# Optimization experiments

Hardware: AMD Instinct MI355X
Metric: run time of the kernel (lower is better)

Reference implementation:

```python
import jax, jax.numpy as jnp
import numpy as np

N = 100000   # nodes
E = 1600000  # edges
F_IN = 128
H = 128
C = 40


def setup_inputs() -> dict:
    key = jax.random.key(0)
    ks = jax.random.split(key, 8)
    x = jax.random.normal(ks[0], (N, F_IN), dtype=jnp.float32)
    edge_index = jax.random.randint(ks[1], (2, E), 0, N, dtype=jnp.int32)
    s_in = 1.0 / np.sqrt(F_IN)
    s_h = 1.0 / np.sqrt(H)
    w0 = jax.random.uniform(ks[2], (F_IN, H), jnp.float32, -s_in, s_in)
    b0 = jnp.zeros((H,), jnp.float32)
    w1 = jax.random.uniform(ks[3], (H, H), jnp.float32, -s_h, s_h)
    b1 = jnp.zeros((H,), jnp.float32)
    wl = jax.random.uniform(ks[4], (H, C), jnp.float32, -s_h, s_h)
    bl = jax.random.uniform(ks[5], (C,), jnp.float32, -s_h, s_h)
    return {"x": x, "edge_index": edge_index, "w0": w0, "b0": b0,
            "w1": w1, "b1": b1, "wl": wl, "bl": bl}


def gcn_conv(x, edge_index, w, b, n):
    # PyG GCNConv: linear transform, add self-loops, D^-1/2 A_hat D^-1/2 aggregation, + bias
    loops = jnp.arange(n, dtype=edge_index.dtype)
    src = jnp.concatenate([edge_index[0], loops])
    dst = jnp.concatenate([edge_index[1], loops])
    deg = jax.ops.segment_sum(jnp.ones_like(dst, dtype=x.dtype), dst, num_segments=n)
    dinv = jnp.where(deg > 0, jax.lax.rsqrt(jnp.maximum(deg, 1.0)), 0.0)
    norm = dinv[src] * dinv[dst]                      # [E+N]
    h = x @ w                                         # [N, out]
    out = jax.ops.segment_sum(norm[:, None] * h[src], dst, num_segments=n)
    return out + b


def reference(x, edge_index, w0, b0, w1, b1, wl, bl):
    # layer 0 (no residual: in/out dims differ conceptually at i==0)
    h = jax.nn.relu(gcn_conv(x, edge_index, w0, b0, N))
    # layer 1 with residual (shapes match); dropout is identity at inference
    h = jax.nn.relu(gcn_conv(h, edge_index, w1, b1, N)) + h
    return jax.nn.log_softmax(h @ wl + bl, axis=1)
```

## Files before the change

### kernel.cpp

```cpp
#include <hip/hip_runtime.h>
#include <math.h>

#define F 128
constexpr int BLK = 256;
constexpr int CAP = 64;

__device__ __forceinline__ unsigned short f2bf(float f) {
    unsigned int b = __float_as_uint(f);
    return (unsigned short)((b + 0x7fffu + ((b >> 16) & 1u)) >> 16);
}


__global__ void bucket_kernel(const int* __restrict__ src, const int* __restrict__ dst, int e,
                              int* __restrict__ counts, int* __restrict__ colb) {
    int i = blockIdx.x * BLK + threadIdx.x;
    if (i < e) {
        int d = dst[i];
        int r = atomicAdd(&counts[d], 1);
        if (r < CAP) colb[d * CAP + r] = src[i];
    }
}

__global__ void dinv_kernel(const int* __restrict__ counts, float* __restrict__ dinv, int n) {
    int i = blockIdx.x * BLK + threadIdx.x;
    if (i < n) dinv[i] = rsqrtf((float)(counts[i] + 1));
}


__global__ __launch_bounds__(256) void mm128_kernel(const float* __restrict__ A,
                                                    const float* __restrict__ W,
                                                    unsigned short* __restrict__ Cb, int n) {
    __shared__ float Ws[64 * 64];
    __shared__ float Xs[64 * 65];
    int t = threadIdx.x;
    int row0 = blockIdx.x * 64;
    int cb = blockIdx.y * 64;
    int r0 = (t & 15) * 4;
    int c0 = (t >> 4) * 4;
    float acc[4][4] = {};

    for (int kt = 0; kt < 2; ++kt) {
        if (kt) __syncthreads();
#pragma unroll
        for (int i = 0; i < 4; i++) {
            int chunk = t + i * 256;
            int k = chunk >> 4;
            int c = (chunk & 15) << 2;
            *(float4*)&Ws[k * 64 + c] = *(const float4*)&W[(kt * 64 + k) * 128 + cb + c];
        }
#pragma unroll
        for (int i = 0; i < 4; i++) {
            int chunk = t + i * 256;
            int r = chunk >> 4;
            int k4 = (chunk & 15) << 2;
            int gr = row0 + r;
            float4 v = (gr < n) ? *(const float4*)&A[(size_t)gr * 128 + kt * 64 + k4]
                                : make_float4(0.f, 0.f, 0.f, 0.f);
            Xs[r * 65 + k4 + 0] = v.x;
            Xs[r * 65 + k4 + 1] = v.y;
            Xs[r * 65 + k4 + 2] = v.z;
            Xs[r * 65 + k4 + 3] = v.w;
        }
        __syncthreads();

#pragma unroll 8
        for (int k = 0; k < 64; ++k) {
            float4 w = *(const float4*)&Ws[k * 64 + c0];
            float x0 = Xs[(r0 + 0) * 65 + k];
            float x1 = Xs[(r0 + 1) * 65 + k];
            float x2 = Xs[(r0 + 2) * 65 + k];
            float x3 = Xs[(r0 + 3) * 65 + k];
            acc[0][0] += x0 * w.x; acc[0][1] += x0 * w.y; acc[0][2] += x0 * w.z; acc[0][3] += x0 * w.w;
            acc[1][0] += x1 * w.x; acc[1][1] += x1 * w.y; acc[1][2] += x1 * w.z; acc[1][3] += x1 * w.w;
            acc[2][0] += x2 * w.x; acc[2][1] += x2 * w.y; acc[2][2] += x2 * w.z; acc[2][3] += x2 * w.w;
            acc[3][0] += x3 * w.x; acc[3][1] += x3 * w.y; acc[3][2] += x3 * w.z; acc[3][3] += x3 * w.w;
        }
    }
#pragma unroll
    for (int m = 0; m < 4; m++) {
        int gr = row0 + r0 + m;
        if (gr < n) {
            ushort4 o;
            o.x = f2bf(acc[m][0]); o.y = f2bf(acc[m][1]);
            o.z = f2bf(acc[m][2]); o.w = f2bf(acc[m][3]);
            *(ushort4*)&Cb[(size_t)gr * 128 + cb + c0] = o;
        }
    }
}


template <bool RESID>
__global__ __launch_bounds__(256) void gather_kernel(const unsigned int* __restrict__ hb,
                                                     const int* __restrict__ cntp,
                                                     const int* __restrict__ colb,
                                                     const float* __restrict__ dinv,
                                                     const float* __restrict__ bias,
                                                     const float* __restrict__ resid,
                                                     float* __restrict__ out, int n) {
    int node = blockIdx.x * 4 + (threadIdx.x >> 6);
    if (node >= n) return;
    int lane = threadIdx.x & 63;

    int cnt = min(cntp[node], CAP);
    int eb = node * CAP;
    float ax = 0.f, ay = 0.f;

    int idx = 0;
    float w = 0.f;
    if (lane < cnt) {
        idx = colb[eb + lane];
        w = dinv[idx];
    }
    int e = 0;
    for (; e + 8 <= cnt; e += 8) {
        int s0 = __shfl(idx, e + 0), s1 = __shfl(idx, e + 1);
        int s2 = __shfl(idx, e + 2), s3 = __shfl(idx, e + 3);
        int s4 = __shfl(idx, e + 4), s5 = __shfl(idx, e + 5);
        int s6 = __shfl(idx, e + 6), s7 = __shfl(idx, e + 7);
        float w0 = __shfl(w, e + 0), w1 = __shfl(w, e + 1);
        float w2 = __shfl(w, e + 2), w3 = __shfl(w, e + 3);
        float w4 = __shfl(w, e + 4), w5 = __shfl(w, e + 5);
        float w6 = __shfl(w, e + 6), w7 = __shfl(w, e + 7);
        unsigned int u0 = hb[(size_t)s0 * 64 + lane];
        unsigned int u1 = hb[(size_t)s1 * 64 + lane];
        unsigned int u2 = hb[(size_t)s2 * 64 + lane];
        unsigned int u3 = hb[(size_t)s3 * 64 + lane];
        unsigned int u4 = hb[(size_t)s4 * 64 + lane];
        unsigned int u5 = hb[(size_t)s5 * 64 + lane];
        unsigned int u6 = hb[(size_t)s6 * 64 + lane];
        unsigned int u7 = hb[(size_t)s7 * 64 + lane];
        ax += w0 * __uint_as_float(u0 << 16); ay += w0 * __uint_as_float(u0 & 0xffff0000u);
        ax += w1 * __uint_as_float(u1 << 16); ay += w1 * __uint_as_float(u1 & 0xffff0000u);
        ax += w2 * __uint_as_float(u2 << 16); ay += w2 * __uint_as_float(u2 & 0xffff0000u);
        ax += w3 * __uint_as_float(u3 << 16); ay += w3 * __uint_as_float(u3 & 0xffff0000u);
        ax += w4 * __uint_as_float(u4 << 16); ay += w4 * __uint_as_float(u4 & 0xffff0000u);
        ax += w5 * __uint_as_float(u5 << 16); ay += w5 * __uint_as_float(u5 & 0xffff0000u);
        ax += w6 * __uint_as_float(u6 << 16); ay += w6 * __uint_as_float(u6 & 0xffff0000u);
        ax += w7 * __uint_as_float(u7 << 16); ay += w7 * __uint_as_float(u7 & 0xffff0000u);
    }
    for (; e < cnt; ++e) {
        int s = __shfl(idx, e);
        float ww = __shfl(w, e);
        unsigned int u = hb[(size_t)s * 64 + lane];
        ax += ww * __uint_as_float(u << 16);
        ay += ww * __uint_as_float(u & 0xffff0000u);
    }

    float di = dinv[node];
    unsigned int us = hb[(size_t)node * 64 + lane];
    ax = di * (ax + di * __uint_as_float(us << 16));
    ay = di * (ay + di * __uint_as_float(us & 0xffff0000u));
    float2 bb = ((const float2*)bias)[lane];
    ax = fmaxf(ax + bb.x, 0.f);
    ay = fmaxf(ay + bb.y, 0.f);
    if (RESID) {
        float2 r = ((const float2*)resid)[(size_t)node * 64 + lane];
        ax += r.x;
        ay += r.y;
    }
    ((float2*)out)[(size_t)node * 64 + lane] = make_float2(ax, ay);
}


__global__ __launch_bounds__(256) void cls_kernel(const float* __restrict__ H,
                                                  const float* __restrict__ WL,
                                                  const float* __restrict__ BL,
                                                  float* __restrict__ out, int n) {
    __shared__ float Hs[64 * 132];
    __shared__ float WsP[128 * 48];
    __shared__ float Bs[40];
    int t = threadIdx.x;
    int n0 = blockIdx.x * 64;

    for (int i = t; i < 128 * 40; i += 256) {
        int k = i / 40;
        int c = i % 40;
        WsP[k * 48 + (c / 10) * 12 + (c % 10)] = WL[i];
    }
    if (t < 40) Bs[t] = BL[t];
#pragma unroll
    for (int i = 0; i < 8; i++) {
        int chunk = t + i * 256;
        int r = chunk >> 5;
        int kk = (chunk & 31) << 2;
        int gr = n0 + r;
        float4 v = (gr < n) ? *(const float4*)&H[(size_t)gr * 128 + kk]
                            : make_float4(0.f, 0.f, 0.f, 0.f);
        *(float4*)&Hs[r * 132 + kk] = v;
    }
    __syncthreads();

    int ln = t >> 2;
    int g = t & 3;
    int node = n0 + ln;
    float acc[10];
#pragma unroll
    for (int j = 0; j < 10; j++) acc[j] = 0.f;

    for (int k4 = 0; k4 < 128; k4 += 4) {
        float4 hv = *(const float4*)&Hs[ln * 132 + k4];
#pragma unroll
        for (int kk = 0; kk < 4; ++kk) {
            const float* wr = &WsP[(k4 + kk) * 48 + g * 12];
            float4 wa = *(const float4*)wr;
            float4 wb = *(const float4*)(wr + 4);
            float2 wc = *(const float2*)(wr + 8);
            float hvk = (&hv.x)[kk];
            acc[0] += hvk * wa.x; acc[1] += hvk * wa.y; acc[2] += hvk * wa.z; acc[3] += hvk * wa.w;
            acc[4] += hvk * wb.x; acc[5] += hvk * wb.y; acc[6] += hvk * wb.z; acc[7] += hvk * wb.w;
            acc[8] += hvk * wc.x; acc[9] += hvk * wc.y;
        }
    }
#pragma unroll
    for (int j = 0; j < 10; j++) acc[j] += Bs[g * 10 + j];

    float m = acc[0];
#pragma unroll
    for (int j = 1; j < 10; j++) m = fmaxf(m, acc[j]);
    m = fmaxf(m, __shfl_xor(m, 1, 64));
    m = fmaxf(m, __shfl_xor(m, 2, 64));
    float ssum = 0.f;
#pragma unroll
    for (int j = 0; j < 10; j++) ssum += expf(acc[j] - m);
    ssum += __shfl_xor(ssum, 1, 64);
    ssum += __shfl_xor(ssum, 2, 64);
    float ls = logf(ssum);

    if (node < n) {
#pragma unroll
        for (int j = 0; j < 10; j++) out[(size_t)node * 40 + g * 10 + j] = acc[j] - m - ls;
    }
}


extern "C" void kernel_launch(void* const* d_in, const int* in_sizes, int n_in,
                              void* d_out, int out_size, void* d_ws, size_t ws_size,
                              hipStream_t stream) {
    const float* x  = (const float*)d_in[0];
    const int*   ei = (const int*)d_in[1];
    const float* w0 = (const float*)d_in[2];
    const float* b0 = (const float*)d_in[3];
    const float* w1 = (const float*)d_in[4];
    const float* b1 = (const float*)d_in[5];
    const float* wl = (const float*)d_in[6];
    const float* bl = (const float*)d_in[7];
    float* out = (float*)d_out;

    int n = in_sizes[0] / F;
    int e = in_sizes[1] / 2;
    const int* src = ei;
    const int* dst = ei + e;

    char* ws = (char*)d_ws;
    size_t off = 0;
    auto alloc = [&](size_t bytes) {
        void* p = ws + off;
        off += (bytes + 255) & ~(size_t)255;
        return p;
    };
    unsigned short* B1b = (unsigned short*)alloc((size_t)n * F * 2);
    float*          B2  = (float*)alloc((size_t)n * F * 4);
    float*          dinv   = (float*)alloc((size_t)n * 4);
    int*            counts = (int*)alloc((size_t)n * 4);
    int*            colb   = (int*)alloc((size_t)n * CAP * 4);
    (void)ws_size;

    int nbN = (n + BLK - 1) / BLK;
    int nbE = (e + BLK - 1) / BLK;
    dim3 mmg((n + 63) / 64, 2);

    hipMemsetAsync(counts, 0, (size_t)n * 4, stream);
    bucket_kernel<<<nbE, BLK, 0, stream>>>(src, dst, e, counts, colb);
    dinv_kernel<<<nbN, BLK, 0, stream>>>(counts, dinv, n);

    mm128_kernel<<<mmg, BLK, 0, stream>>>(x, w0, B1b, n);
    gather_kernel<false><<<(n + 3) / 4, BLK, 0, stream>>>((const unsigned int*)B1b, counts, colb,
                                                          dinv, b0, nullptr, B2, n);
    mm128_kernel<<<mmg, BLK, 0, stream>>>(B2, w1, B1b, n);
    gather_kernel<true><<<(n + 3) / 4, BLK, 0, stream>>>((const unsigned int*)B1b, counts, colb,
                                                         dinv, b1, B2, B2, n);
    cls_kernel<<<(n + 63) / 64, BLK, 0, stream>>>(B2, wl, bl, out, n);
}
```

Measured before the change: 529.9 us.

## Fuse edge bucketing with first matmul and compute dinv inline in gather

```diff
diff --git a/kernel.cpp b/kernel.cpp
--- a/kernel.cpp
+++ b/kernel.cpp
@@ -11,19 +11,82 @@
 }
 
 
-__global__ void bucket_kernel(const int* __restrict__ src, const int* __restrict__ dst, int e,
-                              int* __restrict__ counts, int* __restrict__ colb) {
-    int i = blockIdx.x * BLK + threadIdx.x;
-    if (i < e) {
-        int d = dst[i];
-        int r = atomicAdd(&counts[d], 1);
-        if (r < CAP) colb[d * CAP + r] = src[i];
-    }
-}
-
-__global__ void dinv_kernel(const int* __restrict__ counts, float* __restrict__ dinv, int n) {
-    int i = blockIdx.x * BLK + threadIdx.x;
-    if (i < n) dinv[i] = rsqrtf((float)(counts[i] + 1));
+__global__ __launch_bounds__(256) void fused_bucket_mm_kernel(
+        const int* __restrict__ src, const int* __restrict__ dst, int e,
+        int* __restrict__ counts, int* __restrict__ colb,
+        const float* __restrict__ A, const float* __restrict__ W,
+        unsigned short* __restrict__ Cb, int n, int nmm) {
+    __shared__ float Ws[64 * 64];
+    __shared__ float Xs[64 * 65];
+    int bid = blockIdx.x;
+    int t = threadIdx.x;
+    int mmCand = bid / 3;
+    bool isMM = (bid % 3 == 0) && (mmCand < nmm);
+
+    if (!isMM) {
+        int bkIdx = bid - min(bid / 3 + 1, nmm);
+        int i = bkIdx * BLK + t;
+        if (i < e) {
+            int d = dst[i];
+            int r = atomicAdd(&counts[d], 1);
+            if (r < CAP) colb[d * CAP + r] = src[i];
+        }
+        return;
+    }
+
+    int row0 = (mmCand >> 1) * 64;
+    int cb = (mmCand & 1) * 64;
+    int r0 = (t & 15) * 4;
+    int c0 = (t >> 4) * 4;
+    float acc[4][4] = {};
+
+    for (int kt = 0; kt < 2; ++kt) {
+        if (kt) __syncthreads();
+#pragma unroll
+        for (int i = 0; i < 4; i++) {
+            int chunk = t + i * 256;
+            int k = chunk >> 4;
+            int c = (chunk & 15) << 2;
+            *(float4*)&Ws[k * 64 + c] = *(const float4*)&W[(kt * 64 + k) * 128 + cb + c];
+        }
+#pragma unroll
+        for (int i = 0; i < 4; i++) {
+            int chunk = t + i * 256;
+            int r = chunk >> 4;
+            int k4 = (chunk & 15) << 2;
+            int gr = row0 + r;
+            float4 v = (gr < n) ? *(const float4*)&A[(size_t)gr * 128 + kt * 64 + k4]
+                                : make_float4(0.f, 0.f, 0.f, 0.f);
+            Xs[r * 65 + k4 + 0] = v.x;
+            Xs[r * 65 + k4 + 1] = v.y;
+            Xs[r * 65 + k4 + 2] = v.z;
+            Xs[r * 65 + k4 + 3] = v.w;
+        }
+        __syncthreads();
+
+#pragma unroll 8
+        for (int k = 0; k < 64; ++k) {
+            float4 w = *(const float4*)&Ws[k * 64 + c0];
+            float x0 = Xs[(r0 + 0) * 65 + k];
+            float x1 = Xs[(r0 + 1) * 65 + k];
+            float x2 = Xs[(r0 + 2) * 65 + k];
+            float x3 = Xs[(r0 + 3) * 65 + k];
+            acc[0][0] += x0 * w.x; acc[0][1] += x0 * w.y; acc[0][2] += x0 * w.z; acc[0][3] += x0 * w.w;
+            acc[1][0] += x1 * w.x; acc[1][1] += x1 * w.y; acc[1][2] += x1 * w.z; acc[1][3] += x1 * w.w;
+            acc[2][0] += x2 * w.x; acc[2][1] += x2 * w.y; acc[2][2] += x2 * w.z; acc[2][3] += x2 * w.w;
+            acc[3][0] += x3 * w.x; acc[3][1] += x3 * w.y; acc[3][2] += x3 * w.z; acc[3][3] += x3 * w.w;
+        }
+    }
+#pragma unroll
+    for (int m = 0; m < 4; m++) {
+        int gr = row0 + r0 + m;
+        if (gr < n) {
+            ushort4 o;
+            o.x = f2bf(acc[m][0]); o.y = f2bf(acc[m][1]);
+            o.z = f2bf(acc[m][2]); o.w = f2bf(acc[m][3]);
+            *(ushort4*)&Cb[(size_t)gr * 128 + cb + c0] = o;
+        }
+    }
 }
 
 
@@ -93,7 +156,6 @@
 __global__ __launch_bounds__(256) void gather_kernel(const unsigned int* __restrict__ hb,
                                                      const int* __restrict__ cntp,
                                                      const int* __restrict__ colb,
-                                                     const float* __restrict__ dinv,
                                                      const float* __restrict__ bias,
                                                      const float* __restrict__ resid,
                                                      float* __restrict__ out, int n) {
@@ -109,7 +171,7 @@
     float w = 0.f;
     if (lane < cnt) {
         idx = colb[eb + lane];
-        w = dinv[idx];
+        w = rsqrtf((float)(cntp[idx] + 1));
     }
     int e = 0;
     for (; e + 8 <= cnt; e += 8) {
@@ -146,7 +208,7 @@
         ay += ww * __uint_as_float(u & 0xffff0000u);
     }
 
-    float di = dinv[node];
+    float di = rsqrtf((float)(cnt + 1));
     unsigned int us = hb[(size_t)node * 64 + lane];
     ax = di * (ax + di * __uint_as_float(us << 16));
     ay = di * (ay + di * __uint_as_float(us & 0xffff0000u));
@@ -260,24 +322,21 @@
     };
     unsigned short* B1b = (unsigned short*)alloc((size_t)n * F * 2);
     float*          B2  = (float*)alloc((size_t)n * F * 4);
-    float*          dinv   = (float*)alloc((size_t)n * 4);
     int*            counts = (int*)alloc((size_t)n * 4);
     int*            colb   = (int*)alloc((size_t)n * CAP * 4);
     (void)ws_size;
 
-    int nbN = (n + BLK - 1) / BLK;
-    int nbE = (e + BLK - 1) / BLK;
+    int nmm = 2 * ((n + 63) / 64);
+    int nbk = (e + BLK - 1) / BLK;
     dim3 mmg((n + 63) / 64, 2);
 
     hipMemsetAsync(counts, 0, (size_t)n * 4, stream);
-    bucket_kernel<<<nbE, BLK, 0, stream>>>(src, dst, e, counts, colb);
-    dinv_kernel<<<nbN, BLK, 0, stream>>>(counts, dinv, n);
-
-    mm128_kernel<<<mmg, BLK, 0, stream>>>(x, w0, B1b, n);
+    fused_bucket_mm_kernel<<<nmm + nbk, BLK, 0, stream>>>(src, dst, e, counts, colb,
+                                                          x, w0, B1b, n, nmm);
     gather_kernel<false><<<(n + 3) / 4, BLK, 0, stream>>>((const unsigned int*)B1b, counts, colb,
-                                                          dinv, b0, nullptr, B2, n);
+                                                          b0, nullptr, B2, n);
     mm128_kernel<<<mmg, BLK, 0, stream>>>(B2, w1, B1b, n);
     gather_kernel<true><<<(n + 3) / 4, BLK, 0, stream>>>((const unsigned int*)B1b, counts, colb,
-                                                         dinv, b1, B2, B2, n);
+                                                         b1, B2, B2, n);
     cls_kernel<<<(n + 63) / 64, BLK, 0, stream>>>(B2, wl, bl, out, n);
 }
```

After: 457.2 us. 1.16x faster.
